# Kernel optimization log

Hardware: AMD Instinct MI355X
Metric: run time of the kernel (lower is better)

The kernel has to match this reference:

```python
import jax, jax.numpy as jnp
import numpy as np

L, B, A, I, H = 128, 128, 512, 512, 1024


def setup_inputs() -> dict:
    key = jax.random.key(0)
    ks = jax.random.split(key, 8)
    s = 0.02
    return {
        "action_features": jax.random.normal(ks[0], (L, B, A), jnp.float32),
        "input_feature": jax.random.normal(ks[1], (B, I), jnp.float32),
        "hidden_state": jax.random.normal(ks[2], (B, H), jnp.float32) * s,
        "state": jax.random.normal(ks[3], (B, H), jnp.float32) * s,
        "W_ih": jax.random.normal(ks[4], (4 * H, I + A), jnp.float32) * s,
        "W_hh": jax.random.normal(ks[5], (4 * H, H), jnp.float32) * s,
        "b_ih": jax.random.normal(ks[6], (4 * H,), jnp.float32) * s,
        "b_hh": jax.random.normal(ks[7], (4 * H,), jnp.float32) * s,
    }


def reference(action_features, input_feature, hidden_state, state, W_ih, W_hh, b_ih, b_hh):
    # x_t = concat(input_feature, a_t); precompute the input-side gate projection
    # for all timesteps in one big GEMM: [L,B,I+A] @ [I+A,4H] -> [L,B,4H]
    x = jnp.concatenate(
        [jnp.broadcast_to(input_feature, (action_features.shape[0],) + input_feature.shape),
         action_features], axis=-1)
    gates_x = jnp.einsum('lbi,gi->lbg', x, W_ih) + b_ih + b_hh

    def step(carry, gx):
        h, c = carry
        gates = gx + h @ W_hh.T  # [B, 4H]
        i_g, f_g, g_g, o_g = jnp.split(gates, 4, axis=-1)
        c1 = jax.nn.sigmoid(f_g) * c + jax.nn.sigmoid(i_g) * jnp.tanh(g_g)
        h1 = jax.nn.sigmoid(o_g) * jnp.tanh(c1)
        return (h1, c1), h1

    (h_n, c_n), hs = jax.lax.scan(step, (hidden_state, state), gates_x)
    return hs, h_n, c_n
```

## Files before the change

kernel.cpp:

```cpp
#include <hip/hip_runtime.h>
#include <hip/hip_bf16.h>

#define LL 128
#define BB 128
#define AA 512
#define II 512
#define HH 1024
#define GG 4096
#define KK 1024
#define NTEAM 8
#define NDG 32
#define NBLK (NTEAM * NDG)

typedef __attribute__((ext_vector_type(8))) short short8;
typedef __attribute__((ext_vector_type(4))) float f32x4;
typedef __attribute__((ext_vector_type(4))) unsigned uint32x4;

static __device__ __forceinline__ unsigned short f2b(float x) {
    union { float f; unsigned u; } v; v.f = x;
    unsigned r = v.u + 0x7fffu + ((v.u >> 16) & 1u);
    return (unsigned short)(r >> 16);
}
static __device__ __forceinline__ float b2f(unsigned short b) {
    union { unsigned u; float f; } v; v.u = ((unsigned)b) << 16; return v.f;
}
static __device__ __forceinline__ float fast_sigmoid(float x) {
    return 1.f / (1.f + __expf(-x));
}
static __device__ __forceinline__ float fast_tanh(float x) {
    float e = __expf(2.f * x);
    return (e - 1.f) / (e + 1.f);
}

typedef const __attribute__((address_space(1))) unsigned char ga_u8;
typedef __attribute__((address_space(3))) unsigned char ls_u8;
static __device__ __forceinline__ void gload_lds16(void* lds_base, const void* gsrc) {
    __builtin_amdgcn_global_load_lds((ga_u8*)gsrc, (ls_u8*)lds_base, 16, 0, 0);
}

static __device__ __forceinline__ short8 uc_load128(const unsigned short* p) {
    short8 r;
    asm volatile("global_load_dwordx4 %0, %1, off sc0 sc1" : "=v"(r) : "v"(p));
    return r;
}
static __device__ __forceinline__ void uc_store128(unsigned short* p, uint32x4 v) {
    asm volatile("global_store_dwordx4 %0, %1, off sc0 sc1" :: "v"(p), "v"(v) : "memory");
}
static __device__ __forceinline__ unsigned uc_flag_load(const unsigned int* p) {
    unsigned fv;
    asm volatile("global_load_dword %0, %1, off sc0 sc1\n\ts_waitcnt vmcnt(0)"
                 : "=v"(fv) : "v"(p) : "memory");
    return fv;
}
static __device__ __forceinline__ void uc_flag_store(unsigned int* p, unsigned v) {
    asm volatile("global_store_dword %0, %1, off sc0 sc1" :: "v"(p), "v"(v) : "memory");
}

__global__ void build_x_kernel(const float* __restrict__ act, const float* __restrict__ inF,
                               unsigned short* __restrict__ xb) {
    int stride = gridDim.x * blockDim.x;
    for (int idx = blockIdx.x * blockDim.x + threadIdx.x; idx < LL * BB * KK; idx += stride) {
        int i  = idx & (KK - 1);
        int lb = idx >> 10;
        float v;
        if (i < II) v = inF[(lb & (BB - 1)) * II + i];
        else        v = act[(size_t)lb * AA + (i - II)];
        xb[idx] = f2b(v);
    }
}

__global__ void cast_kernel(const float* __restrict__ s, unsigned short* __restrict__ d, int n) {
    int stride = gridDim.x * blockDim.x;
    for (int i = blockIdx.x * blockDim.x + threadIdx.x; i < n; i += stride) d[i] = f2b(s[i]);
}

__launch_bounds__(256)
__global__ void gemm_x_kernel(const unsigned short* __restrict__ Ab,
                              const unsigned short* __restrict__ Bb,
                              unsigned short* __restrict__ Cb) {
    __shared__ __attribute__((aligned(16))) unsigned short As[128 * 32];
    __shared__ __attribute__((aligned(16))) unsigned short Bs[128 * 32];
    const int tid  = threadIdx.x;
    const int lane = tid & 63;
    const int wid  = tid >> 6;
    const int wr = wid >> 1, wc = wid & 1;
    const int m0 = blockIdx.x * 128, n0 = blockIdx.y * 128;
    const int lrow = lane & 15, lko = (lane >> 4) * 8;
    f32x4 acc[4][4] = {};

    for (int kt = 0; kt < KK / 32; ++kt) {
        const int k0 = kt * 32;
        #pragma unroll
        for (int t = 0; t < 2; ++t) {
            int q   = t * 256 + tid;
            int row = q >> 2;
            int co  = (q & 3) * 8;
            gload_lds16(&As[(t * 256 + wid * 64) * 8], &Ab[(size_t)(m0 + row) * KK + k0 + co]);
            gload_lds16(&Bs[(t * 256 + wid * 64) * 8], &Bb[(size_t)(n0 + row) * KK + k0 + co]);
        }
        __syncthreads();
        short8 af[4], bf[4];
        #pragma unroll
        for (int mi = 0; mi < 4; ++mi)
            af[mi] = *(const short8*)&As[(wr * 64 + mi * 16 + lrow) * 32 + lko];
        #pragma unroll
        for (int ni = 0; ni < 4; ++ni)
            bf[ni] = *(const short8*)&Bs[(wc * 64 + ni * 16 + lrow) * 32 + lko];
        #pragma unroll
        for (int mi = 0; mi < 4; ++mi)
            #pragma unroll
            for (int ni = 0; ni < 4; ++ni)
                acc[mi][ni] = __builtin_amdgcn_mfma_f32_16x16x32_bf16(af[mi], bf[ni], acc[mi][ni], 0, 0, 0);
        __syncthreads();
    }
    #pragma unroll
    for (int mi = 0; mi < 4; ++mi) {
        #pragma unroll
        for (int ni = 0; ni < 4; ++ni) {
            int col = n0 + wc * 64 + ni * 16 + lrow;
            #pragma unroll
            for (int r = 0; r < 4; ++r) {
                int row = m0 + wr * 64 + mi * 16 + (lane >> 4) * 4 + r;
                Cb[(size_t)row * GG + col] = f2b(acc[mi][ni][r]);
            }
        }
    }
}

__launch_bounds__(512, 2)
__global__ void lstm_kernel(const unsigned short* __restrict__ gx,
                            const float* __restrict__ Whh,
                            const float* __restrict__ bih,
                            const float* __restrict__ bhh,
                            const float* __restrict__ c0,
                            unsigned short* __restrict__ hb,
                            unsigned int* __restrict__ flagsG,
                            float* __restrict__ out) {
    __shared__ float red[2 * 3 * 64 * 17];
    __shared__ __attribute__((aligned(16))) unsigned short hbuf[16 * 32];

    const int tid  = threadIdx.x;
    const int lane = tid & 63;
    const int w    = tid >> 6;
    const int nq   = w >> 2;
    const int ksl  = w & 3;
    const int dg   = blockIdx.x & (NDG - 1);
    const int mg   = blockIdx.x >> 5;
    const int j0   = dg * 32;
    const int b0   = mg * 16;
    const int d    = lane & 15;
    const int rg   = lane >> 4;

    short8 breg[4][8];
    #pragma unroll
    for (int t = 0; t < 4; ++t) {
        #pragma unroll
        for (int kf = 0; kf < 8; ++kf) {
            const float* src = &Whh[(size_t)(t * HH + j0 + nq * 16 + d) * HH + ksl * 256 + kf * 32 + rg * 8];
            short8 v;
            #pragma unroll
            for (int j = 0; j < 8; ++j) v[j] = (short)f2b(src[j]);
            breg[t][kf] = v;
        }
    }

    float bias_r[4], c_r[4];
    if (ksl == 0) {
        #pragma unroll
        for (int t = 0; t < 4; ++t)
            bias_r[t] = bih[t * HH + j0 + nq * 16 + d] + bhh[t * HH + j0 + nq * 16 + d];
        #pragma unroll
        for (int r = 0; r < 4; ++r) c_r[r] = c0[(b0 + rg * 4 + r) * HH + j0 + nq * 16 + d];
    }

    unsigned int*       ourflag  = flagsG + mg * NDG + dg;
    const unsigned int* pollflag = flagsG + mg * NDG + (lane & 31);

    for (int l = 0; l < LL; ++l) {
        const unsigned short* hr = hb + (size_t)(l & 1) * (BB * HH);
        unsigned short*       hw = hb + (size_t)((l + 1) & 1) * (BB * HH);

        float gxv[4][4];
        if (ksl == 0) {
            #pragma unroll
            for (int r = 0; r < 4; ++r) {
                const unsigned short* gp = &gx[((size_t)l * BB + (b0 + rg * 4 + r)) * GG + j0 + nq * 16 + d];
                #pragma unroll
                for (int t = 0; t < 4; ++t) gxv[r][t] = b2f(gp[t * HH]);
            }
        }

        if (l > 0 && w == 7) {
            unsigned fv; int guard = 0;
            do { fv = uc_flag_load(pollflag); }
            while (__any(fv < (unsigned)l) && ++guard < (1 << 18));
        }
        __syncthreads();

        short8 af[8];
        const unsigned short* hp = hr + (size_t)(b0 + d) * HH + ksl * 256 + rg * 8;
        #pragma unroll
        for (int kf = 0; kf < 8; ++kf) af[kf] = uc_load128(hp + kf * 32);
        asm volatile("s_waitcnt vmcnt(0)" ::: "memory");
        __builtin_amdgcn_sched_barrier(0);

        f32x4 acc[4] = {};
        #pragma unroll
        for (int kf = 0; kf < 8; ++kf)
            #pragma unroll
            for (int t = 0; t < 4; ++t)
                acc[t] = __builtin_amdgcn_mfma_f32_16x16x32_bf16(af[kf], breg[t][kf], acc[t], 0, 0, 0);

        if (ksl != 0) {
            float* sp = &red[(size_t)((nq * 3 + (ksl - 1)) * 64 + lane) * 17];
            #pragma unroll
            for (int t = 0; t < 4; ++t)
                #pragma unroll
                for (int r = 0; r < 4; ++r) sp[t * 4 + r] = acc[t][r];
        }
        __syncthreads();

        if (ksl == 0) {
            #pragma unroll
            for (int s = 0; s < 3; ++s) {
                const float* sp = &red[(size_t)((nq * 3 + s) * 64 + lane) * 17];
                #pragma unroll
                for (int t = 0; t < 4; ++t)
                    #pragma unroll
                    for (int r = 0; r < 4; ++r) acc[t][r] += sp[t * 4 + r];
            }
            #pragma unroll
            for (int r = 0; r < 4; ++r) {
                float gi = acc[0][r] + gxv[r][0] + bias_r[0];
                float gf = acc[1][r] + gxv[r][1] + bias_r[1];
                float gg = acc[2][r] + gxv[r][2] + bias_r[2];
                float go = acc[3][r] + gxv[r][3] + bias_r[3];
                float ig = fast_sigmoid(gi);
                float fg = fast_sigmoid(gf);
                float og = fast_sigmoid(go);
                float gt = fast_tanh(gg);
                float c1 = fg * c_r[r] + ig * gt;
                float h1 = og * fast_tanh(c1);
                c_r[r] = c1;
                hbuf[(rg * 4 + r) * 32 + nq * 16 + d] = f2b(h1);
                out[((size_t)l * BB + (b0 + rg * 4 + r)) * HH + j0 + nq * 16 + d] = h1;
                if (l == LL - 1) {
                    out[(size_t)LL * BB * HH + (b0 + rg * 4 + r) * HH + j0 + nq * 16 + d] = h1;
                    out[(size_t)LL * BB * HH + BB * HH + (b0 + rg * 4 + r) * HH + j0 + nq * 16 + d] = c1;
                }
            }
        }
        __syncthreads();

        if (w == 2) {
            int row = lane >> 2, ch = lane & 3;
            uint32x4 hv = *(const uint32x4*)&hbuf[row * 32 + ch * 8];
            uc_store128(&hw[(size_t)(b0 + row) * HH + j0 + ch * 8], hv);
            asm volatile("s_waitcnt vmcnt(0)" ::: "memory");
            if (lane == 0) uc_flag_store(ourflag, (unsigned)(l + 1));
        }
    }
}

extern "C" void kernel_launch(void* const* d_in, const int* in_sizes, int n_in,
                              void* d_out, int out_size, void* d_ws, size_t ws_size,
                              hipStream_t stream) {
    const float* act = (const float*)d_in[0];
    const float* inF = (const float*)d_in[1];
    const float* h0  = (const float*)d_in[2];
    const float* c0  = (const float*)d_in[3];
    const float* Wih = (const float*)d_in[4];
    const float* Whh = (const float*)d_in[5];
    const float* bih = (const float*)d_in[6];
    const float* bhh = (const float*)d_in[7];
    float* out = (float*)d_out;

    char* p = (char*)d_ws;
    unsigned short* xb    = (unsigned short*)p; p += (size_t)LL * BB * KK * 2;
    unsigned short* wih_b = (unsigned short*)p; p += (size_t)GG * KK * 2;
    unsigned short* hb    = (unsigned short*)p; p += (size_t)2 * BB * HH * 2;
    unsigned short* gx    = (unsigned short*)p; p += (size_t)LL * BB * GG * 2;
    unsigned int*   flags = (unsigned int*)p;   p += NTEAM * NDG * sizeof(unsigned int);

    hipMemsetAsync(flags, 0, NTEAM * NDG * sizeof(unsigned int), stream);
    build_x_kernel<<<dim3(2048), dim3(256), 0, stream>>>(act, inF, xb);
    cast_kernel<<<dim3(1024), dim3(256), 0, stream>>>(Wih, wih_b, GG * KK);
    cast_kernel<<<dim3(64), dim3(256), 0, stream>>>(h0, hb, BB * HH);
    gemm_x_kernel<<<dim3(128, 32), dim3(256), 0, stream>>>(xb, wih_b, gx);

    void* args[] = { (void*)&gx, (void*)&Whh, (void*)&bih, (void*)&bhh,
                     (void*)&c0, (void*)&hb, (void*)&flags, (void*)&out };
    hipLaunchCooperativeKernel((const void*)lstm_kernel, dim3(NBLK), dim3(512), args, 0, stream);
}
```

Before: 949.7 us.

## Fuse input projection into recurrent LSTM kernel, hoisting time-invariant input_feature term

Removes the separate build_x and large gx GEMM kernels and the bf16 gx round-trip through memory. The input_feature half of the input projection is constant across timesteps, so each block computes it once at startup and folds it into a per-thread bias. The action half is computed inside each timestep with MFMA, using W_ih slices cached in LDS. This puts extra MFMA work and LDS reads on the sequential critical path, and raises LDS use per block, which could affect the two-blocks-per-CU occupancy.

Measured after the change: 789.9 us. -16.8%, faster.

```diff
diff --git a/kernel.cpp b/kernel.cpp
--- a/kernel.cpp
+++ b/kernel.cpp
@@ -21,21 +21,12 @@
     unsigned r = v.u + 0x7fffu + ((v.u >> 16) & 1u);
     return (unsigned short)(r >> 16);
 }
-static __device__ __forceinline__ float b2f(unsigned short b) {
-    union { unsigned u; float f; } v; v.u = ((unsigned)b) << 16; return v.f;
-}
 static __device__ __forceinline__ float fast_sigmoid(float x) {
     return 1.f / (1.f + __expf(-x));
 }
 static __device__ __forceinline__ float fast_tanh(float x) {
     float e = __expf(2.f * x);
     return (e - 1.f) / (e + 1.f);
-}
-
-typedef const __attribute__((address_space(1))) unsigned char ga_u8;
-typedef __attribute__((address_space(3))) unsigned char ls_u8;
-static __device__ __forceinline__ void gload_lds16(void* lds_base, const void* gsrc) {
-    __builtin_amdgcn_global_load_lds((ga_u8*)gsrc, (ls_u8*)lds_base, 16, 0, 0);
 }
 
 static __device__ __forceinline__ short8 uc_load128(const unsigned short* p) {
@@ -56,79 +47,15 @@
     asm volatile("global_store_dword %0, %1, off sc0 sc1" :: "v"(p), "v"(v) : "memory");
 }
 
-__global__ void build_x_kernel(const float* __restrict__ act, const float* __restrict__ inF,
-                               unsigned short* __restrict__ xb) {
-    int stride = gridDim.x * blockDim.x;
-    for (int idx = blockIdx.x * blockDim.x + threadIdx.x; idx < LL * BB * KK; idx += stride) {
-        int i  = idx & (KK - 1);
-        int lb = idx >> 10;
-        float v;
-        if (i < II) v = inF[(lb & (BB - 1)) * II + i];
-        else        v = act[(size_t)lb * AA + (i - II)];
-        xb[idx] = f2b(v);
-    }
-}
-
 __global__ void cast_kernel(const float* __restrict__ s, unsigned short* __restrict__ d, int n) {
     int stride = gridDim.x * blockDim.x;
     for (int i = blockIdx.x * blockDim.x + threadIdx.x; i < n; i += stride) d[i] = f2b(s[i]);
 }
 
-__launch_bounds__(256)
-__global__ void gemm_x_kernel(const unsigned short* __restrict__ Ab,
-                              const unsigned short* __restrict__ Bb,
-                              unsigned short* __restrict__ Cb) {
-    __shared__ __attribute__((aligned(16))) unsigned short As[128 * 32];
-    __shared__ __attribute__((aligned(16))) unsigned short Bs[128 * 32];
-    const int tid  = threadIdx.x;
-    const int lane = tid & 63;
-    const int wid  = tid >> 6;
-    const int wr = wid >> 1, wc = wid & 1;
-    const int m0 = blockIdx.x * 128, n0 = blockIdx.y * 128;
-    const int lrow = lane & 15, lko = (lane >> 4) * 8;
-    f32x4 acc[4][4] = {};
-
-    for (int kt = 0; kt < KK / 32; ++kt) {
-        const int k0 = kt * 32;
-        #pragma unroll
-        for (int t = 0; t < 2; ++t) {
-            int q   = t * 256 + tid;
-            int row = q >> 2;
-            int co  = (q & 3) * 8;
-            gload_lds16(&As[(t * 256 + wid * 64) * 8], &Ab[(size_t)(m0 + row) * KK + k0 + co]);
-            gload_lds16(&Bs[(t * 256 + wid * 64) * 8], &Bb[(size_t)(n0 + row) * KK + k0 + co]);
-        }
-        __syncthreads();
-        short8 af[4], bf[4];
-        #pragma unroll
-        for (int mi = 0; mi < 4; ++mi)
-            af[mi] = *(const short8*)&As[(wr * 64 + mi * 16 + lrow) * 32 + lko];
-        #pragma unroll
-        for (int ni = 0; ni < 4; ++ni)
-            bf[ni] = *(const short8*)&Bs[(wc * 64 + ni * 16 + lrow) * 32 + lko];
-        #pragma unroll
-        for (int mi = 0; mi < 4; ++mi)
-            #pragma unroll
-            for (int ni = 0; ni < 4; ++ni)
-                acc[mi][ni] = __builtin_amdgcn_mfma_f32_16x16x32_bf16(af[mi], bf[ni], acc[mi][ni], 0, 0, 0);
-        __syncthreads();
-    }
-    #pragma unroll
-    for (int mi = 0; mi < 4; ++mi) {
-        #pragma unroll
-        for (int ni = 0; ni < 4; ++ni) {
-            int col = n0 + wc * 64 + ni * 16 + lrow;
-            #pragma unroll
-            for (int r = 0; r < 4; ++r) {
-                int row = m0 + wr * 64 + mi * 16 + (lane >> 4) * 4 + r;
-                Cb[(size_t)row * GG + col] = f2b(acc[mi][ni][r]);
-            }
-        }
-    }
-}
-
 __launch_bounds__(512, 2)
-__global__ void lstm_kernel(const unsigned short* __restrict__ gx,
+__global__ void lstm_kernel(const unsigned short* __restrict__ xa,
+                            const float* __restrict__ inF,
+                            const float* __restrict__ Wih,
                             const float* __restrict__ Whh,
                             const float* __restrict__ bih,
                             const float* __restrict__ bhh,
@@ -136,6 +63,7 @@
                             unsigned short* __restrict__ hb,
                             unsigned int* __restrict__ flagsG,
                             float* __restrict__ out) {
+    __shared__ __attribute__((aligned(16))) unsigned short wa_lds[8 * 16 * 64 * 8];
     __shared__ float red[2 * 3 * 64 * 17];
     __shared__ __attribute__((aligned(16))) unsigned short hbuf[16 * 32];
 
@@ -164,14 +92,61 @@
         }
     }
 
-    float bias_r[4], c_r[4];
+    #pragma unroll
+    for (int t = 0; t < 4; ++t) {
+        #pragma unroll
+        for (int kf = 0; kf < 4; ++kf) {
+            const float* src = &Wih[(size_t)(t * HH + j0 + nq * 16 + d) * KK + II + ksl * 128 + kf * 32 + rg * 8];
+            unsigned short* dst = &wa_lds[(((size_t)w * 16 + t * 4 + kf) * 64 + lane) * 8];
+            #pragma unroll
+            for (int j = 0; j < 8; ++j) dst[j] = f2b(src[j]);
+        }
+    }
+
+    f32x4 bacc[4] = {};
+    #pragma unroll
+    for (int kf = 0; kf < 4; ++kf) {
+        const float* xs = &inF[(size_t)(b0 + d) * II + ksl * 128 + kf * 32 + rg * 8];
+        short8 xf;
+        #pragma unroll
+        for (int j = 0; j < 8; ++j) xf[j] = (short)f2b(xs[j]);
+        #pragma unroll
+        for (int t = 0; t < 4; ++t) {
+            const float* ws = &Wih[(size_t)(t * HH + j0 + nq * 16 + d) * KK + ksl * 128 + kf * 32 + rg * 8];
+            short8 wf;
+            #pragma unroll
+            for (int j = 0; j < 8; ++j) wf[j] = (short)f2b(ws[j]);
+            bacc[t] = __builtin_amdgcn_mfma_f32_16x16x32_bf16(xf, wf, bacc[t], 0, 0, 0);
+        }
+    }
+    if (ksl != 0) {
+        float* sp = &red[(size_t)((nq * 3 + (ksl - 1)) * 64 + lane) * 17];
+        #pragma unroll
+        for (int t = 0; t < 4; ++t)
+            #pragma unroll
+            for (int r = 0; r < 4; ++r) sp[t * 4 + r] = bacc[t][r];
+    }
+    __syncthreads();
+    float base_r[16], c_r[4];
     if (ksl == 0) {
         #pragma unroll
-        for (int t = 0; t < 4; ++t)
-            bias_r[t] = bih[t * HH + j0 + nq * 16 + d] + bhh[t * HH + j0 + nq * 16 + d];
+        for (int s = 0; s < 3; ++s) {
+            const float* sp = &red[(size_t)((nq * 3 + s) * 64 + lane) * 17];
+            #pragma unroll
+            for (int t = 0; t < 4; ++t)
+                #pragma unroll
+                for (int r = 0; r < 4; ++r) bacc[t][r] += sp[t * 4 + r];
+        }
+        #pragma unroll
+        for (int t = 0; t < 4; ++t) {
+            float bias = bih[t * HH + j0 + nq * 16 + d] + bhh[t * HH + j0 + nq * 16 + d];
+            #pragma unroll
+            for (int r = 0; r < 4; ++r) base_r[t * 4 + r] = bacc[t][r] + bias;
+        }
         #pragma unroll
         for (int r = 0; r < 4; ++r) c_r[r] = c0[(b0 + rg * 4 + r) * HH + j0 + nq * 16 + d];
     }
+    __syncthreads();
 
     unsigned int*       ourflag  = flagsG + mg * NDG + dg;
     const unsigned int* pollflag = flagsG + mg * NDG + (lane & 31);
@@ -180,14 +155,19 @@
         const unsigned short* hr = hb + (size_t)(l & 1) * (BB * HH);
         unsigned short*       hw = hb + (size_t)((l + 1) & 1) * (BB * HH);
 
-        float gxv[4][4];
-        if (ksl == 0) {
-            #pragma unroll
-            for (int r = 0; r < 4; ++r) {
-                const unsigned short* gp = &gx[((size_t)l * BB + (b0 + rg * 4 + r)) * GG + j0 + nq * 16 + d];
-                #pragma unroll
-                for (int t = 0; t < 4; ++t) gxv[r][t] = b2f(gp[t * HH]);
-            }
+        f32x4 acc[4] = {};
+        {
+            const unsigned short* ap = xa + ((size_t)l * BB + b0 + d) * AA + ksl * 128 + rg * 8;
+            short8 aaf[4];
+            #pragma unroll
+            for (int kf = 0; kf < 4; ++kf) aaf[kf] = *(const short8*)(ap + kf * 32);
+            #pragma unroll
+            for (int kf = 0; kf < 4; ++kf)
+                #pragma unroll
+                for (int t = 0; t < 4; ++t) {
+                    short8 wfr = *(const short8*)&wa_lds[(((size_t)w * 16 + t * 4 + kf) * 64 + lane) * 8];
+                    acc[t] = __builtin_amdgcn_mfma_f32_16x16x32_bf16(aaf[kf], wfr, acc[t], 0, 0, 0);
+                }
         }
 
         if (l > 0 && w == 7) {
@@ -204,7 +184,6 @@
         asm volatile("s_waitcnt vmcnt(0)" ::: "memory");
         __builtin_amdgcn_sched_barrier(0);
 
-        f32x4 acc[4] = {};
         #pragma unroll
         for (int kf = 0; kf < 8; ++kf)
             #pragma unroll
@@ -231,10 +210,10 @@
             }
             #pragma unroll
             for (int r = 0; r < 4; ++r) {
-                float gi = acc[0][r] + gxv[r][0] + bias_r[0];
-                float gf = acc[1][r] + gxv[r][1] + bias_r[1];
-                float gg = acc[2][r] + gxv[r][2] + bias_r[2];
-                float go = acc[3][r] + gxv[r][3] + bias_r[3];
+                float gi = acc[0][r] + base_r[0 + r];
+                float gf = acc[1][r] + base_r[4 + r];
+                float gg = acc[2][r] + base_r[8 + r];
+                float go = acc[3][r] + base_r[12 + r];
                 float ig = fast_sigmoid(gi);
                 float fg = fast_sigmoid(gf);
                 float og = fast_sigmoid(go);
@@ -276,19 +255,15 @@
     float* out = (float*)d_out;
 
     char* p = (char*)d_ws;
-    unsigned short* xb    = (unsigned short*)p; p += (size_t)LL * BB * KK * 2;
-    unsigned short* wih_b = (unsigned short*)p; p += (size_t)GG * KK * 2;
+    unsigned short* xa    = (unsigned short*)p; p += (size_t)LL * BB * AA * 2;
     unsigned short* hb    = (unsigned short*)p; p += (size_t)2 * BB * HH * 2;
-    unsigned short* gx    = (unsigned short*)p; p += (size_t)LL * BB * GG * 2;
     unsigned int*   flags = (unsigned int*)p;   p += NTEAM * NDG * sizeof(unsigned int);
 
     hipMemsetAsync(flags, 0, NTEAM * NDG * sizeof(unsigned int), stream);
-    build_x_kernel<<<dim3(2048), dim3(256), 0, stream>>>(act, inF, xb);
-    cast_kernel<<<dim3(1024), dim3(256), 0, stream>>>(Wih, wih_b, GG * KK);
+    cast_kernel<<<dim3(2048), dim3(256), 0, stream>>>(act, xa, LL * BB * AA);
     cast_kernel<<<dim3(64), dim3(256), 0, stream>>>(h0, hb, BB * HH);
-    gemm_x_kernel<<<dim3(128, 32), dim3(256), 0, stream>>>(xb, wih_b, gx);
-
-    void* args[] = { (void*)&gx, (void*)&Whh, (void*)&bih, (void*)&bhh,
-                     (void*)&c0, (void*)&hb, (void*)&flags, (void*)&out };
+
+    void* args[] = { (void*)&xa, (void*)&inF, (void*)&Wih, (void*)&Whh, (void*)&bih,
+                     (void*)&bhh, (void*)&c0, (void*)&hb, (void*)&flags, (void*)&out };
     hipLaunchCooperativeKernel((const void*)lstm_kernel, dim3(NBLK), dim3(512), args, 0, stream);
 }
```
